# Optimization experiments

Hardware: AMD Instinct MI355X
Metric: run time of the kernel (lower is better)

Reference implementation:

```python
import jax, jax.numpy as jnp
import numpy as np

B, CS, CT, H, W = 16, 512, 512, 64, 64

def setup_inputs() -> dict:
    key = jax.random.key(0)
    k1, k2 = jax.random.split(key)
    x = jax.random.normal(k1, (B, CS, H, W), dtype=jnp.float32)
    # 16 Linear weights, each [out_ch, in_ch] (torch Linear layout), stacked
    Wg = jax.random.normal(k2, (16, CT, CS), dtype=jnp.float32) * (2.0 / CT) ** 0.5
    return {"x": x, "Wg": Wg}

def reference(x, Wg):
    # x: [B, Cs, H, W]; Wg: [16, Ct, Cs] indexed by phase r*4+c, r=(i%4), c=(j%4)
    # Dropout is identity in eval mode (deterministic reference).
    b, cs, h, w = x.shape
    ct = Wg.shape[1]
    Wrq = Wg.reshape(4, 4, ct, cs)               # [r, q, Ct, Cs]
    xr = x.reshape(b, cs, h // 4, 4, w // 4, 4)  # [b, c, h4, r, w4, q]
    # grouped matmul: each (r,q) phase uses its own weight
    out = jnp.einsum('bchrwq,rqoc->bohrwq', xr, Wrq)
    return out.reshape(b, ct, h, w)
```

## Files before the change

### kernel.cpp

```cpp
#include <hip/hip_runtime.h>
#include <stdint.h>


typedef __attribute__((ext_vector_type(8))) short short8;
typedef __attribute__((ext_vector_type(4))) float f32x4;

#define CS 512
#define CT 512
#define HW 4096
#define BK 32
#define MT 64
#define BPITCH 40

__device__ __forceinline__ uint16_t f32_to_bf16(float f) {
    uint32_t u = __builtin_bit_cast(uint32_t, f);
    u += 0x7FFFu + ((u >> 16) & 1u);
    return (uint16_t)(u >> 16);
}

__global__ __launch_bounds__(256)
void w2_cvt(const float* __restrict__ Wg, uint16_t* __restrict__ W2) {
    int idx = (blockIdx.x * 256 + threadIdx.x) * 8;
    float4 a = *(const float4*)(Wg + idx);
    float4 b = *(const float4*)(Wg + idx + 4);
    uint16_t o[8];
    o[0]=f32_to_bf16(a.x); o[1]=f32_to_bf16(a.y); o[2]=f32_to_bf16(a.z); o[3]=f32_to_bf16(a.w);
    o[4]=f32_to_bf16(b.x); o[5]=f32_to_bf16(b.y); o[6]=f32_to_bf16(b.z); o[7]=f32_to_bf16(b.w);
    *(short8*)(W2 + idx) = *(short8*)o;
}

template<bool USE_W2>
__global__ __launch_bounds__(256, 3)
void gwl_main(const float* __restrict__ x, const float* __restrict__ Wg,
              const uint16_t* __restrict__ W2, float* __restrict__ out) {
    const int nb = blockIdx.x;
    const int mb = blockIdx.y;
    const int r  = blockIdx.z;
    const int m0 = mb * MT;

    __shared__ __align__(16) unsigned char smem[36864];
    uint16_t* As = (uint16_t*)smem;
    uint16_t* Bs = (uint16_t*)(smem + 16384);
    float*    T  = (float*)smem;

    const int tid  = threadIdx.x;
    const int lane = tid & 63;
    const int wave = tid >> 6;
    const int lr = lane & 15, qd = lane >> 4;

    const int w16 = tid & 15;
    const int rho = (tid >> 4) & 3;
    const int kw  = tid >> 6;
    const int rg  = nb * 4 + rho;
    const int bb  = rg >> 4;
    const int h4  = rg & 15;
    const float* bbase = x + (size_t)bb * CS * HW
                           + (size_t)((h4 * 4 + r) * 64 + w16 * 4);

    const uint16_t* abase = USE_W2
        ? W2 + ((size_t)(r * 4 + wave) * CT + m0) * CS : (const uint16_t*)nullptr;

    float4 breg[8];
    auto loadB = [&](int k0) {
        const float* p = bbase + (size_t)(k0 + kw * 8) * HW;
        #pragma unroll
        for (int cc = 0; cc < 8; ++cc) breg[cc] = *(const float4*)(p + (size_t)cc * HW);
    };
    auto writeB = [&]() {
        #pragma unroll
        for (int q = 0; q < 4; ++q) {
            uint16_t tmp[8];
            #pragma unroll
            for (int cc = 0; cc < 8; ++cc)
                tmp[cc] = f32_to_bf16(((const float*)&breg[cc])[q]);
            *(short8*)(Bs + (q * 64 + rho * 16 + w16) * BPITCH + kw * 8) = *(short8*)tmp;
        }
    };
    auto stageA_glds = [&](int k0) {
        #pragma unroll
        for (int t = 0; t < 4; ++t) {
            const uint16_t* src = abase + (size_t)(t * 16 + (lane >> 2)) * CS
                                        + k0 + (lane & 3) * 8;
            uint16_t* dst = As + wave * 2048 + t * 512;
            __builtin_amdgcn_global_load_lds(
                (const __attribute__((address_space(1))) void*)src,
                (__attribute__((address_space(3))) void*)dst, 16, 0, 0);
        }
    };
    auto stageA_fp32 = [&](int k0) {
        const int qa = tid >> 6, rem = tid & 63;
        const int ka = rem & 7, ma = rem >> 3;
        const float* ap = Wg + ((size_t)(r * 4 + qa) * CT + m0 + ma) * CS + k0 + ka * 4;
        #pragma unroll
        for (int it = 0; it < 8; ++it) {
            float4 v = *(const float4*)(ap + (size_t)it * 8 * CS);
            uint16_t tmp[4] = {f32_to_bf16(v.x), f32_to_bf16(v.y),
                               f32_to_bf16(v.z), f32_to_bf16(v.w)};
            *(uint64_t*)(As + qa * 2048 + (ma + it * 8) * 32 + ka * 4) =
                *(const uint64_t*)tmp;
        }
    };

    f32x4 acc[4][4] = {};

    loadB(0);
    if (USE_W2) stageA_glds(0); else stageA_fp32(0);
    writeB();
    loadB(BK);

    const uint16_t* Asq = As + wave * 2048;
    const uint16_t* Bsq = Bs + wave * 64 * BPITCH;

    for (int k = 0; k < 16; ++k) {
        __syncthreads();
        short8 afr[4], bfr[4];
        #pragma unroll
        for (int i = 0; i < 4; ++i)
            afr[i] = *(const short8*)(Asq + (i * 16 + lr) * 32 + qd * 8);
        #pragma unroll
        for (int j = 0; j < 4; ++j)
            bfr[j] = *(const short8*)(Bsq + (j * 16 + lr) * BPITCH + qd * 8);
        if (k < 15) {
            __syncthreads();
            if (USE_W2) stageA_glds((k + 1) * BK); else stageA_fp32((k + 1) * BK);
            writeB();
            if (k < 14) loadB((k + 2) * BK);
        }
        #pragma unroll
        for (int i = 0; i < 4; ++i)
            #pragma unroll
            for (int j = 0; j < 4; ++j)
                acc[i][j] = __builtin_amdgcn_mfma_f32_16x16x32_bf16(
                    afr[i], bfr[j], acc[i][j], 0, 0, 0);
    }

    const int q = wave;
    const int m16s = tid >> 4;
    const int rs   = (tid >> 2) & 3;
    const int ws   = (tid & 3) * 16;
    const int rgs  = nb * 4 + rs;
    const int obb  = rgs >> 4;
    const int oh4  = rgs & 15;
    #pragma unroll
    for (int ic = 0; ic < 4; ++ic) {
        __syncthreads();
        #pragma unroll
        for (int j = 0; j < 4; ++j)
            #pragma unroll
            for (int g = 0; g < 4; ++g)
                T[((qd * 4 + g) * 4 + j) * 68 + lr * 4 + q] = acc[ic][j][g];
        __syncthreads();
        float* op = out + ((size_t)obb * CT + m0 + ic * 16 + m16s) * HW
                        + (oh4 * 4 + r) * 64 + ws;
        const float* tp = T + (m16s * 4 + rs) * 68 + ws;
        #pragma unroll
        for (int c = 0; c < 4; ++c)
            ((float4*)op)[c] = ((const float4*)tp)[c];
    }
}

extern "C" void kernel_launch(void* const* d_in, const int* in_sizes, int n_in,
                              void* d_out, int out_size, void* d_ws, size_t ws_size,
                              hipStream_t stream) {
    const float* x  = (const float*)d_in[0];
    const float* Wg = (const float*)d_in[1];
    float* out = (float*)d_out;
    dim3 grid(64, 8, 4);
    if (ws_size >= (size_t)16 * 512 * 512 * 2) {
        uint16_t* W2 = (uint16_t*)d_ws;
        w2_cvt<<<2048, 256, 0, stream>>>(Wg, W2);
        gwl_main<true><<<grid, 256, 0, stream>>>(x, Wg, W2, out);
    } else {
        gwl_main<false><<<grid, 256, 0, stream>>>(x, Wg, nullptr, out);
    }
}
```

Before: 320.7 us.

## Double block tile to 128 channels by 8 row-groups with 512 threads and swizzled A LDS

Each block now covers 128 output channels and 8 row-groups per phase row, using 8 waves and a larger LDS allocation. The grid shrinks fourfold, so every staged A and B tile is reused across more MFMAs and global traffic per output falls. The A tile in LDS also gets an XOR swizzle on its k-chunks to cut bank conflicts on fragment reads. In exchange the kernel holds a 4x8 accumulator array, which raises register pressure and may lower occupancy, and the grid has only 512 blocks.

```diff
diff --git a/kernel.cpp b/kernel.cpp
--- a/kernel.cpp
+++ b/kernel.cpp
@@ -9,7 +9,8 @@
 #define CT 512
 #define HW 4096
 #define BK 32
-#define MT 64
+#define MT 128
+#define NR 8
 #define BPITCH 40
 
 __device__ __forceinline__ uint16_t f32_to_bf16(float f) {
@@ -30,7 +31,7 @@
 }
 
 template<bool USE_W2>
-__global__ __launch_bounds__(256, 3)
+__global__ __launch_bounds__(512, 2)
 void gwl_main(const float* __restrict__ x, const float* __restrict__ Wg,
               const uint16_t* __restrict__ W2, float* __restrict__ out) {
     const int nb = blockIdx.x;
@@ -38,27 +39,29 @@
     const int r  = blockIdx.z;
     const int m0 = mb * MT;
 
-    __shared__ __align__(16) unsigned char smem[36864];
+    __shared__ __align__(16) unsigned char smem[73728];
     uint16_t* As = (uint16_t*)smem;
-    uint16_t* Bs = (uint16_t*)(smem + 16384);
+    uint16_t* Bs = (uint16_t*)(smem + 32768);
     float*    T  = (float*)smem;
 
     const int tid  = threadIdx.x;
     const int lane = tid & 63;
     const int wave = tid >> 6;
+    const int q    = wave & 3;
+    const int mw   = wave >> 2;
     const int lr = lane & 15, qd = lane >> 4;
 
     const int w16 = tid & 15;
-    const int rho = (tid >> 4) & 3;
-    const int kw  = tid >> 6;
-    const int rg  = nb * 4 + rho;
+    const int rho = (tid >> 4) & 7;
+    const int kw  = tid >> 7;
+    const int rg  = nb * NR + rho;
     const int bb  = rg >> 4;
     const int h4  = rg & 15;
     const float* bbase = x + (size_t)bb * CS * HW
                            + (size_t)((h4 * 4 + r) * 64 + w16 * 4);
 
     const uint16_t* abase = USE_W2
-        ? W2 + ((size_t)(r * 4 + wave) * CT + m0) * CS : (const uint16_t*)nullptr;
+        ? W2 + ((size_t)(r * 4 + q) * CT + m0 + mw * 64) * CS : (const uint16_t*)nullptr;
 
     float4 breg[8];
     auto loadB = [&](int k0) {
@@ -68,57 +71,58 @@
     };
     auto writeB = [&]() {
         #pragma unroll
-        for (int q = 0; q < 4; ++q) {
+        for (int qq = 0; qq < 4; ++qq) {
             uint16_t tmp[8];
             #pragma unroll
             for (int cc = 0; cc < 8; ++cc)
-                tmp[cc] = f32_to_bf16(((const float*)&breg[cc])[q]);
-            *(short8*)(Bs + (q * 64 + rho * 16 + w16) * BPITCH + kw * 8) = *(short8*)tmp;
+                tmp[cc] = f32_to_bf16(((const float*)&breg[cc])[qq]);
+            *(short8*)(Bs + (qq * 128 + rho * 16 + w16) * BPITCH + kw * 8) = *(short8*)tmp;
         }
     };
     auto stageA_glds = [&](int k0) {
         #pragma unroll
         for (int t = 0; t < 4; ++t) {
             const uint16_t* src = abase + (size_t)(t * 16 + (lane >> 2)) * CS
-                                        + k0 + (lane & 3) * 8;
-            uint16_t* dst = As + wave * 2048 + t * 512;
+                                        + k0 + (((lane & 3) ^ ((lane >> 2) & 3)) * 8);
+            uint16_t* dst = As + (q * 128 + mw * 64) * 32 + t * 512;
             __builtin_amdgcn_global_load_lds(
                 (const __attribute__((address_space(1))) void*)src,
                 (__attribute__((address_space(3))) void*)dst, 16, 0, 0);
         }
     };
     auto stageA_fp32 = [&](int k0) {
-        const int qa = tid >> 6, rem = tid & 63;
+        const int qa = tid >> 7, rem = tid & 127;
         const int ka = rem & 7, ma = rem >> 3;
         const float* ap = Wg + ((size_t)(r * 4 + qa) * CT + m0 + ma) * CS + k0 + ka * 4;
+        const int kc = (((ka >> 1) ^ (ma & 3)) * 8) + (ka & 1) * 4;
         #pragma unroll
         for (int it = 0; it < 8; ++it) {
-            float4 v = *(const float4*)(ap + (size_t)it * 8 * CS);
+            float4 v = *(const float4*)(ap + (size_t)it * 16 * CS);
             uint16_t tmp[4] = {f32_to_bf16(v.x), f32_to_bf16(v.y),
                                f32_to_bf16(v.z), f32_to_bf16(v.w)};
-            *(uint64_t*)(As + qa * 2048 + (ma + it * 8) * 32 + ka * 4) =
+            *(uint64_t*)(As + (qa * 128 + ma + it * 16) * 32 + kc) =
                 *(const uint64_t*)tmp;
         }
     };
 
-    f32x4 acc[4][4] = {};
+    f32x4 acc[4][8] = {};
 
     loadB(0);
     if (USE_W2) stageA_glds(0); else stageA_fp32(0);
     writeB();
     loadB(BK);
 
-    const uint16_t* Asq = As + wave * 2048;
-    const uint16_t* Bsq = Bs + wave * 64 * BPITCH;
+    const uint16_t* Asq = As + (q * 128 + mw * 64) * 32;
+    const uint16_t* Bsq = Bs + q * 128 * BPITCH;
 
     for (int k = 0; k < 16; ++k) {
         __syncthreads();
-        short8 afr[4], bfr[4];
+        short8 afr[4], bfr[8];
         #pragma unroll
         for (int i = 0; i < 4; ++i)
-            afr[i] = *(const short8*)(Asq + (i * 16 + lr) * 32 + qd * 8);
+            afr[i] = *(const short8*)(Asq + (i * 16 + lr) * 32 + ((qd ^ (lr & 3)) * 8));
         #pragma unroll
-        for (int j = 0; j < 4; ++j)
+        for (int j = 0; j < 8; ++j)
             bfr[j] = *(const short8*)(Bsq + (j * 16 + lr) * BPITCH + qd * 8);
         if (k < 15) {
             __syncthreads();
@@ -129,30 +133,32 @@
         #pragma unroll
         for (int i = 0; i < 4; ++i)
             #pragma unroll
-            for (int j = 0; j < 4; ++j)
+            for (int j = 0; j < 8; ++j)
                 acc[i][j] = __builtin_amdgcn_mfma_f32_16x16x32_bf16(
                     afr[i], bfr[j], acc[i][j], 0, 0, 0);
     }
 
-    const int q = wave;
-    const int m16s = tid >> 4;
-    const int rs   = (tid >> 2) & 3;
+    const int m16s = tid >> 5;
+    const int rs   = (tid >> 2) & 7;
     const int ws   = (tid & 3) * 16;
-    const int rgs  = nb * 4 + rs;
+    const int rgs  = nb * NR + rs;
     const int obb  = rgs >> 4;
     const int oh4  = rgs & 15;
     #pragma unroll
-    for (int ic = 0; ic < 4; ++ic) {
+    for (int ic = 0; ic < 8; ++ic) {
         __syncthreads();
-        #pragma unroll
-        for (int j = 0; j < 4; ++j)
+        if (mw == (ic >> 2)) {
+            const int i = ic & 3;
             #pragma unroll
-            for (int g = 0; g < 4; ++g)
-                T[((qd * 4 + g) * 4 + j) * 68 + lr * 4 + q] = acc[ic][j][g];
+            for (int j = 0; j < 8; ++j)
+                #pragma unroll
+                for (int g = 0; g < 4; ++g)
+                    T[((qd * 4 + g) * 8 + j) * 68 + lr * 4 + q] = acc[i][j][g];
+        }
         __syncthreads();
         float* op = out + ((size_t)obb * CT + m0 + ic * 16 + m16s) * HW
                         + (oh4 * 4 + r) * 64 + ws;
-        const float* tp = T + (m16s * 4 + rs) * 68 + ws;
+        const float* tp = T + (m16s * 8 + rs) * 68 + ws;
         #pragma unroll
         for (int c = 0; c < 4; ++c)
             ((float4*)op)[c] = ((const float4*)tp)[c];
@@ -165,12 +171,12 @@
     const float* x  = (const float*)d_in[0];
     const float* Wg = (const float*)d_in[1];
     float* out = (float*)d_out;
-    dim3 grid(64, 8, 4);
+    dim3 grid(32, 4, 4);
     if (ws_size >= (size_t)16 * 512 * 512 * 2) {
         uint16_t* W2 = (uint16_t*)d_ws;
         w2_cvt<<<2048, 256, 0, stream>>>(Wg, W2);
-        gwl_main<true><<<grid, 256, 0, stream>>>(x, Wg, W2, out);
+        gwl_main<true><<<grid, 512, 0, stream>>>(x, Wg, W2, out);
     } else {
-        gwl_main<false><<<grid, 256, 0, stream>>>(x, Wg, nullptr, out);
+        gwl_main<false><<<grid, 512, 0, stream>>>(x, Wg, nullptr, out);
     }
 }
```

Result: no change. 314.5 us (-1.9%).
